# Optimization experiments

Hardware: AMD Instinct MI355X
Metric: run time of the kernel (lower is better)

Reference implementation:

```python
import jax, jax.numpy as jnp
import numpy as np

B, T, D_MODEL, N_HEADS = 2, 2048, 1024, 16


def setup_inputs() -> dict:
    key = jax.random.key(0)
    ks = jax.random.split(key, 5)
    w_scale = 0.02
    return {
        "x": jax.random.normal(ks[0], (B, T, D_MODEL), jnp.float32),
        "Wq": jax.random.normal(ks[1], (D_MODEL, D_MODEL), jnp.float32) * w_scale,
        "Wk": jax.random.normal(ks[2], (D_MODEL, D_MODEL), jnp.float32) * w_scale,
        "Wv": jax.random.normal(ks[3], (D_MODEL, D_MODEL), jnp.float32) * w_scale,
        "Wo": jax.random.normal(ks[4], (D_MODEL, D_MODEL), jnp.float32) * w_scale,
    }


def reference(x, Wq, Wk, Wv, Wo):
    Bv, Tv, _ = x.shape
    H = N_HEADS
    D = D_MODEL // H
    # Projections (torch nn.Linear: y = x @ W.T), split heads -> (B, H, T, D)
    q = (x @ Wq.T).reshape(Bv, Tv, H, D).transpose(0, 2, 1, 3)
    k = (x @ Wk.T).reshape(Bv, Tv, H, D).transpose(0, 2, 1, 3)
    v = (x @ Wv.T).reshape(Bv, Tv, H, D).transpose(0, 2, 1, 3)

    scale = jnp.sqrt(jnp.asarray(D, jnp.float32))
    scores = jnp.einsum("bhqd,bhkd->bhqk", q, k) / scale  # (B, H, T, T)

    # ALiBi bias: -|i-j| * slope_h, future positions masked to -inf (causal)
    slopes = jnp.asarray(
        [2.0 ** (-8.0 * h / H) for h in range(1, H + 1)], jnp.float32
    )
    pos = jnp.arange(Tv)
    dist = jnp.abs(pos[None, :] - pos[:, None]).astype(jnp.float32)  # (T, T)
    bias = -dist[None, :, :] * slopes[:, None, None]                 # (H, T, T)
    causal_mask = jnp.triu(jnp.ones((Tv, Tv), dtype=bool), 1)
    bias = jnp.where(causal_mask[None, :, :], -jnp.inf, bias)
    scores = scores + bias[None]  # (B, H, T, T)

    attn = jax.nn.softmax(scores, axis=-1)
    out = jnp.einsum("bhqk,bhkd->bhqd", attn, v)
    out = out.transpose(0, 2, 1, 3).reshape(Bv, Tv, D_MODEL)
    return out @ Wo.T
```

## Files before the change

### kernel.cpp

```cpp
#include <hip/hip_runtime.h>


#define DEV __device__ __forceinline__

typedef __attribute__((ext_vector_type(8))) short short8;
typedef __attribute__((ext_vector_type(4))) float f32x4;
typedef __attribute__((ext_vector_type(16))) float f32x16;
typedef __attribute__((ext_vector_type(4))) unsigned short ushort4v;
typedef __attribute__((ext_vector_type(4))) unsigned uint4v;

DEV unsigned short f2bf(float f) {
  unsigned u = __builtin_bit_cast(unsigned, f);
  u += 0x7fffu + ((u >> 16) & 1u);
  return (unsigned short)(u >> 16);
}
DEV float bf2f(unsigned short u) {
  unsigned x = ((unsigned)u) << 16;
  return __builtin_bit_cast(float, x);
}
DEV unsigned cvtpk_bf(float lo, float hi) {
  unsigned r;
  asm("v_cvt_pk_bf16_f32 %0, %1, %2" : "=v"(r) : "v"(lo), "v"(hi));
  return r;
}

DEV void gl2lds16(const void* g, void* l) {
  __builtin_amdgcn_global_load_lds(
      (const __attribute__((address_space(1))) void*)g,
      (__attribute__((address_space(3))) void*)l, 16, 0, 0);
}

__global__ __launch_bounds__(256) void cvt_all(
    const float* __restrict__ x, const float* __restrict__ wq,
    const float* __restrict__ wk, const float* __restrict__ wv,
    const float* __restrict__ wo, unsigned short* __restrict__ xb,
    unsigned short* __restrict__ wqb, unsigned short* __restrict__ wkb,
    unsigned short* __restrict__ wvb, unsigned short* __restrict__ wob) {
  int b = blockIdx.x;
  const float* s;
  unsigned short* d;
  int off;
  if (b < 4096)      { s = x;  d = xb;  off = b; }
  else if (b < 5120) { s = wq; d = wqb; off = b - 4096; }
  else if (b < 6144) { s = wk; d = wkb; off = b - 5120; }
  else if (b < 7168) { s = wv; d = wvb; off = b - 6144; }
  else               { s = wo; d = wob; off = b - 7168; }
  int i = (off * 256 + threadIdx.x) * 4;
  float4 v = *(const float4*)(s + i);
  ushort4v o = {f2bf(v.x), f2bf(v.y), f2bf(v.z), f2bf(v.w)};
  *(ushort4v*)(d + i) = o;
}

__global__ __launch_bounds__(512, 2) void gemm_qkv(
    const unsigned short* __restrict__ A, const unsigned short* __restrict__ Wq,
    const unsigned short* __restrict__ Wk, const unsigned short* __restrict__ Wv,
    unsigned short* __restrict__ Qo, unsigned short* __restrict__ Ko,
    unsigned short* __restrict__ Vo) {
  constexpr int K = 1024;
  __shared__ alignas(16) unsigned short Sm[65536];
  const int t = threadIdx.x;
  const int w = t >> 6, l = t & 63, l15 = l & 15, l4 = l >> 4;
  const int wr = w >> 2, wc = w & 3;
  const int wsel = blockIdx.x >> 2;
  const int n0 = (blockIdx.x & 3) * 256;
  const int m0 = blockIdx.y * 256;
  const unsigned short* Bmat = (wsel == 0) ? Wq : ((wsel == 1) ? Wk : Wv);

  const int srow = t >> 3;
  const int sk = ((t & 7) ^ (srow & 7)) * 8;

#define STG_A(T, H)                                                           \
  {                                                                           \
    gl2lds16(A + (m0 + (H)*128 + srow) * K + (T)*64 + sk,                     \
             &Sm[((T)&1) * 16384 + (H)*8192 + t * 8]);                        \
    gl2lds16(A + (m0 + (H)*128 + 64 + srow) * K + (T)*64 + sk,                \
             &Sm[((T)&1) * 16384 + (H)*8192 + 4096 + t * 8]);                 \
  }
#define STG_B(T, H)                                                           \
  {                                                                           \
    gl2lds16(Bmat + (n0 + (H)*128 + srow) * K + (T)*64 + sk,                  \
             &Sm[32768 + ((T)&1) * 16384 + (H)*8192 + t * 8]);                \
    gl2lds16(Bmat + (n0 + (H)*128 + 64 + srow) * K + (T)*64 + sk,             \
             &Sm[32768 + ((T)&1) * 16384 + (H)*8192 + 4096 + t * 8]);         \
  }

  f32x4 acc[8][4];
  {
    f32x4 z4 = {0.f, 0.f, 0.f, 0.f};
#pragma unroll
    for (int i = 0; i < 8; i++)
#pragma unroll
      for (int j = 0; j < 4; j++) acc[i][j] = z4;
  }
  short8 af[4][2], bf[2][2][2];

#define RD_AF(TT, QM)                                                         \
  {                                                                           \
    const unsigned short* Ab_ = &Sm[((TT)&1) * 16384];                        \
    _Pragma("unroll") for (int mi_ = 0; mi_ < 4; mi_++) {                     \
      _Pragma("unroll") for (int kk_ = 0; kk_ < 2; kk_++) {                   \
        af[mi_][kk_] = *(const short8*)&Ab_[                                  \
            (wr * 128 + (QM)*64 + mi_ * 16 + l15) * 64 +                      \
            (((kk_ * 4 + l4) ^ (l15 & 7)) * 8)];                              \
      }                                                                       \
    }                                                                         \
  }
#define RD_BF(TT, QN)                                                         \
  {                                                                           \
    const unsigned short* Bb_ = &Sm[32768 + ((TT)&1) * 16384];                \
    _Pragma("unroll") for (int ni_ = 0; ni_ < 2; ni_++) {                     \
      _Pragma("unroll") for (int kk_ = 0; kk_ < 2; kk_++) {                   \
        bf[(QN)][ni_][kk_] = *(const short8*)&Bb_[                            \
            (wc * 64 + (QN)*32 + ni_ * 16 + l15) * 64 +                       \
            (((kk_ * 4 + l4) ^ (l15 & 7)) * 8)];                              \
      }                                                                       \
    }                                                                         \
  }
#define DO_MFMA(QM, QN)                                                       \
  {                                                                           \
    _Pragma("unroll") for (int mi_ = 0; mi_ < 4; mi_++) {                     \
      _Pragma("unroll") for (int ni_ = 0; ni_ < 2; ni_++) {                   \
        _Pragma("unroll") for (int kk_ = 0; kk_ < 2; kk_++) {                 \
          acc[(QM)*4 + mi_][(QN)*2 + ni_] =                                   \
              __builtin_amdgcn_mfma_f32_16x16x32_bf16(                        \
                  af[mi_][kk_], bf[(QN)][ni_][kk_],                           \
                  acc[(QM)*4 + mi_][(QN)*2 + ni_], 0, 0, 0);                  \
        }                                                                     \
      }                                                                       \
    }                                                                         \
  }

#define VMW4 asm volatile("s_waitcnt vmcnt(4)" ::: "memory")
#define VMW0 asm volatile("s_waitcnt vmcnt(0)" ::: "memory")
#define NOW ((void)0)
#define PHASE(RDS, STG, MFMA_, WAIT)                                          \
  {                                                                           \
    RDS;                                                                      \
    STG;                                                                      \
    __builtin_amdgcn_sched_barrier(0);                                        \
    __builtin_amdgcn_s_barrier();                                             \
    __builtin_amdgcn_s_setprio(1);                                            \
    MFMA_;                                                                    \
    __builtin_amdgcn_s_setprio(0);                                            \
    __builtin_amdgcn_sched_barrier(0);                                        \
    WAIT;                                                                     \
    __builtin_amdgcn_s_barrier();                                             \
  }

  STG_B(0, 0); STG_B(0, 1); STG_A(0, 0); STG_A(0, 1);
  STG_B(1, 0); STG_B(1, 1);
  VMW4;
  __builtin_amdgcn_sched_barrier(0);
  __builtin_amdgcn_s_barrier();

#pragma unroll 1
  for (int i = 0; i < 7; ++i) {
    const int TA = 2 * i, TB = TA + 1;
    PHASE(RD_AF(TA, 0); RD_BF(TA, 0), STG_A(TB, 0),     DO_MFMA(0, 0), NOW);
    PHASE(RD_BF(TA, 1),               STG_A(TB, 1),     DO_MFMA(0, 1), NOW);
    PHASE(RD_AF(TA, 1),               STG_B(TA + 2, 0), DO_MFMA(1, 0), NOW);
    PHASE(NOW,                        STG_B(TA + 2, 1), DO_MFMA(1, 1), VMW4);
    PHASE(RD_AF(TB, 0); RD_BF(TB, 0), STG_A(TA + 2, 0), DO_MFMA(0, 0), NOW);
    PHASE(RD_BF(TB, 1),               STG_A(TA + 2, 1), DO_MFMA(0, 1), NOW);
    PHASE(RD_AF(TB, 1),               STG_B(TB + 2, 0), DO_MFMA(1, 0), NOW);
    PHASE(NOW,                        STG_B(TB + 2, 1), DO_MFMA(1, 1), VMW4);
  }
  PHASE(RD_AF(14, 0); RD_BF(14, 0), STG_A(15, 0), DO_MFMA(0, 0), NOW);
  PHASE(RD_BF(14, 1),               STG_A(15, 1), DO_MFMA(0, 1), NOW);
  PHASE(RD_AF(14, 1),               NOW,          DO_MFMA(1, 0), NOW);
  PHASE(NOW,                        NOW,          DO_MFMA(1, 1), VMW0);
  PHASE(RD_AF(15, 0); RD_BF(15, 0), NOW,          DO_MFMA(0, 0), NOW);
  PHASE(RD_BF(15, 1),               NOW,          DO_MFMA(0, 1), NOW);
  PHASE(RD_AF(15, 1),               NOW,          DO_MFMA(1, 0), NOW);
  PHASE(NOW,                        NOW,          DO_MFMA(1, 1), NOW);

#undef PHASE
#undef NOW
#undef VMW0
#undef VMW4
#undef DO_MFMA
#undef RD_BF
#undef RD_AF
#undef STG_B
#undef STG_A

  if (wsel != 2) {
    unsigned short* D = (wsel == 0) ? Qo : Ko;
    const float scale = (wsel == 0) ? 0.18033688011112042f : 1.0f;
    const int zb = (n0 >> 6) + wc;
#pragma unroll
    for (int mi = 0; mi < 8; mi++)
#pragma unroll
      for (int r = 0; r < 4; r++) {
        int m = m0 + wr * 128 + mi * 16 + l4 * 4 + r;
        int b = m >> 11, tt = m & 2047;
        int z = b * 16 + zb;
#pragma unroll
        for (int ni = 0; ni < 4; ni++)
          D[(z * 2048 + tt) * 64 + ni * 16 + l15] = f2bf(acc[mi][ni][r] * scale);
      }
  } else {
    unsigned short* Tr = Sm + w * 4608;
    const int b = (m0 + wr * 128) >> 11, tbase = (m0 + wr * 128) & 2047;
    const int zg = b * 16 + (n0 >> 6) + wc;
#pragma unroll
    for (int p = 0; p < 2; p++) {
#pragma unroll
      for (int mi = 0; mi < 4; mi++)
#pragma unroll
        for (int ni = 0; ni < 4; ni++) {
          int mg = p * 4 + mi;
          ushort4v pk = {f2bf(acc[mg][ni][0]), f2bf(acc[mg][ni][1]),
                         f2bf(acc[mg][ni][2]), f2bf(acc[mg][ni][3])};
          *(ushort4v*)&Tr[(ni * 16 + l15) * 72 + mi * 16 + l4 * 4] = pk;
        }
      asm volatile("s_waitcnt lgkmcnt(0)" ::: "memory");
      __builtin_amdgcn_sched_barrier(0);
#pragma unroll
      for (int j = 0; j < 8; j++) {
        int idx = j * 64 + l;
        int d = idx >> 3, c = idx & 7;
        int t0 = (c >> 1) * 16 + (c & 1) * 4;
        ushort4v lo4 = *(const ushort4v*)&Tr[d * 72 + t0];
        ushort4v hi4 = *(const ushort4v*)&Tr[d * 72 + t0 + 8];
        short8 v = {(short)lo4[0], (short)lo4[1], (short)lo4[2], (short)lo4[3],
                    (short)hi4[0], (short)hi4[1], (short)hi4[2], (short)hi4[3]};
        *(short8*)&Vo[(zg * 64 + d) * 2048 + tbase + p * 64 + c * 8] = v;
      }
      asm volatile("s_waitcnt lgkmcnt(0)" ::: "memory");
      __builtin_amdgcn_sched_barrier(0);
    }
  }
}

__global__ __launch_bounds__(256, 2) void gemm_o(
    const unsigned short* __restrict__ A, const unsigned short* __restrict__ Bm,
    float* __restrict__ C) {
  constexpr int K = 1024;
  __shared__ alignas(16) unsigned short Al[128 * 32];
  __shared__ alignas(16) unsigned short Bl[64 * 32];
  const int t = threadIdx.x;
  const int l = t & 63, l15 = l & 15, l4 = l >> 4;
  const int wm = ((t >> 6) & 1) * 64, wn = (t >> 7) * 32;
  const int sblk = (blockIdx.x & 7) * 64 + (blockIdx.x >> 3);
  const int m0 = (sblk >> 4) * 128, n0 = (sblk & 15) * 64;

  f32x4 zero4 = {0.f, 0.f, 0.f, 0.f};
  f32x4 acc[4][2];
#pragma unroll
  for (int i = 0; i < 4; i++)
#pragma unroll
    for (int j = 0; j < 2; j++) acc[i][j] = zero4;

  const int row0 = t >> 2, seg = (t & 3) * 8;
  const unsigned short* Ag0 = A + (m0 + row0) * K + seg;
  const unsigned short* Ag1 = A + (m0 + row0 + 64) * K + seg;
  const unsigned short* Bg0 = Bm + (n0 + row0) * K + seg;

  for (int k0 = 0; k0 < K; k0 += 32) {
    gl2lds16(Ag0 + k0, &Al[t * 8]);
    gl2lds16(Ag1 + k0, &Al[2048 + t * 8]);
    gl2lds16(Bg0 + k0, &Bl[t * 8]);
    __syncthreads();
    short8 af[4], bf2[2];
#pragma unroll
    for (int mi = 0; mi < 4; mi++)
      af[mi] = *(const short8*)&Al[(wm + mi * 16 + l15) * 32 + l4 * 8];
#pragma unroll
    for (int ni = 0; ni < 2; ni++)
      bf2[ni] = *(const short8*)&Bl[(wn + ni * 16 + l15) * 32 + l4 * 8];
#pragma unroll
    for (int mi = 0; mi < 4; mi++)
#pragma unroll
      for (int ni = 0; ni < 2; ni++)
        acc[mi][ni] = __builtin_amdgcn_mfma_f32_16x16x32_bf16(
            af[mi], bf2[ni], acc[mi][ni], 0, 0, 0);
    __syncthreads();
  }
#pragma unroll
  for (int mi = 0; mi < 4; mi++)
#pragma unroll
    for (int r = 0; r < 4; r++) {
      int m = m0 + wm + mi * 16 + l4 * 4 + r;
      float* cp = C + m * 1024 + n0 + wn + l15;
      cp[0] = acc[mi][0][r];
      cp[16] = acc[mi][1][r];
    }
}

__global__ __launch_bounds__(256, 3) void flash_alibi(
    const unsigned short* __restrict__ Q, const unsigned short* __restrict__ Kb,
    const unsigned short* __restrict__ Vt, unsigned short* __restrict__ O0,
    unsigned short* __restrict__ O1, float* __restrict__ L0,
    float* __restrict__ L1) {
  __shared__ alignas(16) unsigned short Kl[2 * 4096];
  __shared__ alignas(16) unsigned short Vl[2 * 4096];
  const int t = threadIdx.x, w = t >> 6, l = t & 63;
  const int l31 = l & 31, h = l >> 5, lsw = l31 & 7;
  const int g = blockIdx.x;
  const int qt = 15 - (g >> 6);
  const int z = (g & 63) >> 1, s = g & 1;
  const int q0 = qt * 128, hd = z & 15;
  const float slope2 = exp2f(-0.5f * (float)(hd + 1)) * 1.4426950408889634f;
  const int qrow = q0 + w * 32;
  const int qi = qrow + l31;

  short8 qf[4];
#pragma unroll
  for (int ks = 0; ks < 4; ks++)
    qf[ks] = *(const short8*)&Q[(z * 2048 + qi) * 64 + ks * 16 + h * 8];

  f32x16 binit;
#pragma unroll
  for (int r = 0; r < 16; r++)
    binit[r] =
        fmaf(slope2, (float)((r & 3) + 8 * (r >> 2) + 4 * h - qi), -10.0f);

  f32x16 accO[2];
  float lsum = 0.f;
#pragma unroll
  for (int nd = 0; nd < 2; nd++)
#pragma unroll
    for (int r = 0; r < 16; r++) accO[nd][r] = 0.f;

  const int sr = t >> 3, sgr = t & 7;
  const int it0 = s ? (qt + 1) : 0;
  const int nt = qt + 1;

#define ISSUE_LOADS(KV0, BUF)                                                 \
  {                                                                           \
    unsigned short* Kd = &Kl[(BUF) * 4096];                                   \
    unsigned short* Vd = &Vl[(BUF) * 4096];                                   \
    const int sx = (sgr ^ (sr & 7)) * 8;                                      \
    gl2lds16(&Kb[(z * 2048 + (KV0) + sr) * 64 + sx], &Kd[t * 8]);             \
    gl2lds16(&Kb[(z * 2048 + (KV0) + 32 + sr) * 64 + sx],                     \
             &Kd[2048 + t * 8]);                                              \
    gl2lds16(&Vt[(z * 64 + sr) * 2048 + (KV0) + sx], &Vd[t * 8]);             \
    gl2lds16(&Vt[(z * 64 + 32 + sr) * 2048 + (KV0) + sx],                     \
             &Vd[2048 + t * 8]);                                              \
  }

  ISSUE_LOADS(it0 * 64, 0)

  for (int ii = 0; ii < nt; ++ii) {
    __syncthreads();
    const int kv0 = (it0 + ii) * 64;
    if (ii + 1 < nt) ISSUE_LOADS(kv0 + 64, (ii + 1) & 1)
    if (kv0 > qrow + 31) continue;
    const unsigned short* Kc = &Kl[(ii & 1) * 4096];
    const unsigned short* Vc = &Vl[(ii & 1) * 4096];

    f32x16 accS[2];
    accS[0] = binit;
    accS[1] = binit;
#pragma unroll
    for (int ks = 0; ks < 4; ks++) {
      short8 kf0 =
          *(const short8*)&Kc[l31 * 64 + (((ks * 2 + h) ^ lsw) * 8)];
      short8 kf1 =
          *(const short8*)&Kc[(32 + l31) * 64 + (((ks * 2 + h) ^ lsw) * 8)];
      accS[0] = __builtin_amdgcn_mfma_f32_32x32x16_bf16(kf0, qf[ks], accS[0],
                                                        0, 0, 0);
      accS[1] = __builtin_amdgcn_mfma_f32_32x32x16_bf16(kf1, qf[ks], accS[1],
                                                        0, 0, 0);
    }

    const bool needMask = (kv0 + 63 > qrow);
#pragma unroll
    for (int ni = 0; ni < 2; ni++) {
      const float fkv = (float)(kv0 + 32 * ni);
      float ps[16];
#pragma unroll
      for (int r = 0; r < 16; r++)
        ps[r] = __builtin_amdgcn_exp2f(fmaf(slope2, fkv, accS[ni][r]));
      if (needMask) {
        const int kb = kv0 + 32 * ni + 4 * h;
#pragma unroll
        for (int r = 0; r < 16; r++)
          if (kb + ((r & 3) + 8 * (r >> 2)) > qi) ps[r] = 0.f;
      }
      lsum += (((ps[0] + ps[1]) + (ps[2] + ps[3])) +
               ((ps[4] + ps[5]) + (ps[6] + ps[7]))) +
              (((ps[8] + ps[9]) + (ps[10] + ps[11])) +
               ((ps[12] + ps[13]) + (ps[14] + ps[15])));
      unsigned pk[8];
#pragma unroll
      for (int i = 0; i < 8; i++) pk[i] = cvtpk_bf(ps[2 * i], ps[2 * i + 1]);
#pragma unroll
      for (int kp = 0; kp < 2; kp++) {
        uint4v pw = {pk[kp * 4 + 0], pk[kp * 4 + 1], pk[kp * 4 + 2],
                     pk[kp * 4 + 3]};
        short8 pa = __builtin_bit_cast(short8, pw);
#pragma unroll
        for (int nd = 0; nd < 2; nd++) {
          short8 vf = *(const short8*)&Vc[(nd * 32 + l31) * 64 +
                                          ((((ni * 2 + kp) * 2 + h) ^ lsw) * 8)];
          accO[nd] = __builtin_amdgcn_mfma_f32_32x32x16_bf16(pa, vf, accO[nd],
                                                             0, 0, 0);
        }
      }
    }
  }
#undef ISSUE_LOADS

  unsigned short* Op = s ? O1 : O0;
  float* Lp = s ? L1 : L0;
  float lv = lsum + __shfl_xor(lsum, 32);
  if (l < 32) Lp[z * 2048 + qrow + l] = lv;
#pragma unroll
  for (int nd = 0; nd < 2; nd++)
#pragma unroll
    for (int r = 0; r < 16; r++) {
      int tg = qrow + (r & 3) + 8 * (r >> 2) + 4 * h;
      Op[(z * 2048 + tg) * 64 + nd * 32 + l31] = f2bf(accO[nd][r]);
    }
}

__global__ __launch_bounds__(256) void combine(
    const unsigned short* __restrict__ O0, const unsigned short* __restrict__ O1,
    const float* __restrict__ L0, const float* __restrict__ L1,
    unsigned short* __restrict__ Ob) {
  int idx = (blockIdx.x * 256 + threadIdx.x) * 8;
  int z = idx >> 17, rem = idx & 131071;
  int tt = rem >> 6, d = rem & 63;
  short8 a = *(const short8*)(O0 + idx);
  short8 b = *(const short8*)(O1 + idx);
  float inv = 1.0f / (L0[z * 2048 + tt] + L1[z * 2048 + tt]);
  short8 o;
#pragma unroll
  for (int j = 0; j < 8; j++) {
    float v = (bf2f((unsigned short)a[j]) + bf2f((unsigned short)b[j])) * inv;
    o[j] = (short)f2bf(v);
  }
  int bq = z >> 4, h = z & 15;
  *(short8*)(Ob + (bq * 2048 + tt) * 1024 + h * 64 + d) = o;
}

extern "C" void kernel_launch(void* const* d_in, const int* in_sizes, int n_in,
                              void* d_out, int out_size, void* d_ws,
                              size_t ws_size, hipStream_t stream) {
  const float* x = (const float*)d_in[0];
  const float* Wq = (const float*)d_in[1];
  const float* Wk = (const float*)d_in[2];
  const float* Wv = (const float*)d_in[3];
  const float* Wo = (const float*)d_in[4];

  char* p = (char*)d_ws;
  unsigned short* xb = (unsigned short*)p;  p += 4096 * 1024 * 2;
  unsigned short* wqb = (unsigned short*)p; p += 1024 * 1024 * 2;
  unsigned short* wkb = (unsigned short*)p; p += 1024 * 1024 * 2;
  unsigned short* wvb = (unsigned short*)p; p += 1024 * 1024 * 2;
  unsigned short* wob = (unsigned short*)p; p += 1024 * 1024 * 2;
  unsigned short* Qb = (unsigned short*)p;  p += 32 * 2048 * 64 * 2;
  unsigned short* Kbf = (unsigned short*)p; p += 32 * 2048 * 64 * 2;
  unsigned short* Vtb = (unsigned short*)p; p += 32 * 2048 * 64 * 2;
  unsigned short* O1 = (unsigned short*)p;  p += 32 * 2048 * 64 * 2;
  float* L0 = (float*)p;                    p += 32 * 2048 * 4;
  float* L1 = (float*)p;                    p += 32 * 2048 * 4;
  unsigned short* O0 = xb;
  unsigned short* Ob = Qb;

  cvt_all<<<8192, 256, 0, stream>>>(x, Wq, Wk, Wv, Wo, xb, wqb, wkb, wvb, wob);
  gemm_qkv<<<dim3(12, 16), 512, 0, stream>>>(xb, wqb, wkb, wvb, Qb, Kbf, Vtb);
  flash_alibi<<<1024, 256, 0, stream>>>(Qb, Kbf, Vtb, O0, O1, L0, L1);
  combine<<<2048, 256, 0, stream>>>(O0, O1, L0, L1, Ob);
  gemm_o<<<512, 256, 0, stream>>>(Ob, wob, (float*)d_out);
}
```

Before: 164.8 us.

## Fuse split-KV combine into output projection GEMM A-tile load

Removes the separate combine kernel and instead merges the two partial attention outputs and normalises them by the summed softmax denominators while loading A tiles inside gemm_o. This drops one launch and one write/read round trip of the combined activation. In exchange, gemm_o now reads two bf16 tiles plus L values per k-step through registers instead of async global-to-LDS copies, and recomputes the division 16 times per row across n-blocks. It also removes the sched_barrier fences in the QKV GEMM phase macro, letting the compiler reorder around the phases.

```diff
diff --git a/kernel.cpp b/kernel.cpp
--- a/kernel.cpp
+++ b/kernel.cpp
@@ -137,12 +137,10 @@
   {                                                                           \
     RDS;                                                                      \
     STG;                                                                      \
-    __builtin_amdgcn_sched_barrier(0);                                        \
     __builtin_amdgcn_s_barrier();                                             \
     __builtin_amdgcn_s_setprio(1);                                            \
     MFMA_;                                                                    \
     __builtin_amdgcn_s_setprio(0);                                            \
-    __builtin_amdgcn_sched_barrier(0);                                        \
     WAIT;                                                                     \
     __builtin_amdgcn_s_barrier();                                             \
   }
@@ -150,7 +148,6 @@
   STG_B(0, 0); STG_B(0, 1); STG_A(0, 0); STG_A(0, 1);
   STG_B(1, 0); STG_B(1, 1);
   VMW4;
-  __builtin_amdgcn_sched_barrier(0);
   __builtin_amdgcn_s_barrier();
 
 #pragma unroll 1
@@ -234,8 +231,9 @@
 }
 
 __global__ __launch_bounds__(256, 2) void gemm_o(
-    const unsigned short* __restrict__ A, const unsigned short* __restrict__ Bm,
-    float* __restrict__ C) {
+    const unsigned short* __restrict__ O0, const unsigned short* __restrict__ O1,
+    const float* __restrict__ L0, const float* __restrict__ L1,
+    const unsigned short* __restrict__ Bm, float* __restrict__ C) {
   constexpr int K = 1024;
   __shared__ alignas(16) unsigned short Al[128 * 32];
   __shared__ alignas(16) unsigned short Bl[64 * 32];
@@ -253,14 +251,33 @@
     for (int j = 0; j < 2; j++) acc[i][j] = zero4;
 
   const int row0 = t >> 2, seg = (t & 3) * 8;
-  const unsigned short* Ag0 = A + (m0 + row0) * K + seg;
-  const unsigned short* Ag1 = A + (m0 + row0 + 64) * K + seg;
+  const int mA0 = m0 + row0, mA1 = m0 + row0 + 64;
+  const int tt0 = mA0 & 2047, bq0 = mA0 >> 11;
+  const int tt1 = mA1 & 2047, bq1 = mA1 >> 11;
   const unsigned short* Bg0 = Bm + (n0 + row0) * K + seg;
 
   for (int k0 = 0; k0 < K; k0 += 32) {
-    gl2lds16(Ag0 + k0, &Al[t * 8]);
-    gl2lds16(Ag1 + k0, &Al[2048 + t * 8]);
+    const int h = k0 >> 6, d0 = (k0 & 32) + seg;
+    const int z0 = bq0 * 16 + h, z1 = bq1 * 16 + h;
+    const int i0 = (z0 * 2048 + tt0) * 64 + d0;
+    const int i1 = (z1 * 2048 + tt1) * 64 + d0;
+    short8 a0 = *(const short8*)(O0 + i0);
+    short8 b0 = *(const short8*)(O1 + i0);
+    short8 a1 = *(const short8*)(O0 + i1);
+    short8 b1 = *(const short8*)(O1 + i1);
+    float inv0 = 1.0f / (L0[z0 * 2048 + tt0] + L1[z0 * 2048 + tt0]);
+    float inv1 = 1.0f / (L0[z1 * 2048 + tt1] + L1[z1 * 2048 + tt1]);
     gl2lds16(Bg0 + k0, &Bl[t * 8]);
+    short8 c0, c1;
+#pragma unroll
+    for (int j = 0; j < 8; j++) {
+      c0[j] = (short)f2bf(
+          (bf2f((unsigned short)a0[j]) + bf2f((unsigned short)b0[j])) * inv0);
+      c1[j] = (short)f2bf(
+          (bf2f((unsigned short)a1[j]) + bf2f((unsigned short)b1[j])) * inv1);
+    }
+    *(short8*)&Al[t * 8] = c0;
+    *(short8*)&Al[2048 + t * 8] = c1;
     __syncthreads();
     short8 af[4], bf2[2];
 #pragma unroll
@@ -416,26 +433,6 @@
     }
 }
 
-__global__ __launch_bounds__(256) void combine(
-    const unsigned short* __restrict__ O0, const unsigned short* __restrict__ O1,
-    const float* __restrict__ L0, const float* __restrict__ L1,
-    unsigned short* __restrict__ Ob) {
-  int idx = (blockIdx.x * 256 + threadIdx.x) * 8;
-  int z = idx >> 17, rem = idx & 131071;
-  int tt = rem >> 6, d = rem & 63;
-  short8 a = *(const short8*)(O0 + idx);
-  short8 b = *(const short8*)(O1 + idx);
-  float inv = 1.0f / (L0[z * 2048 + tt] + L1[z * 2048 + tt]);
-  short8 o;
-#pragma unroll
-  for (int j = 0; j < 8; j++) {
-    float v = (bf2f((unsigned short)a[j]) + bf2f((unsigned short)b[j])) * inv;
-    o[j] = (short)f2bf(v);
-  }
-  int bq = z >> 4, h = z & 15;
-  *(short8*)(Ob + (bq * 2048 + tt) * 1024 + h * 64 + d) = o;
-}
-
 extern "C" void kernel_launch(void* const* d_in, const int* in_sizes, int n_in,
                               void* d_out, int out_size, void* d_ws,
                               size_t ws_size, hipStream_t stream) {
@@ -458,11 +455,9 @@
   float* L0 = (float*)p;                    p += 32 * 2048 * 4;
   float* L1 = (float*)p;                    p += 32 * 2048 * 4;
   unsigned short* O0 = xb;
-  unsigned short* Ob = Qb;
 
   cvt_all<<<8192, 256, 0, stream>>>(x, Wq, Wk, Wv, Wo, xb, wqb, wkb, wvb, wob);
   gemm_qkv<<<dim3(12, 16), 512, 0, stream>>>(xb, wqb, wkb, wvb, Qb, Kbf, Vtb);
   flash_alibi<<<1024, 256, 0, stream>>>(Qb, Kbf, Vtb, O0, O1, L0, L1);
-  combine<<<2048, 256, 0, stream>>>(O0, O1, L0, L1, Ob);
-  gemm_o<<<512, 256, 0, stream>>>(Ob, wob, (float*)d_out);
-}
+  gemm_o<<<512, 256, 0, stream>>>(O0, O1, L0, L1, wob, (float*)d_out);
+}
```

New measurement: 174.8 us. 6.0% more time.
